# Kernel optimization log

Hardware: AMD Instinct MI355X
Metric: run time of the kernel (lower is better)

Reference implementation:

```python
import jax, jax.numpy as jnp
import numpy as np

B, CIN, H, W = 8, 128, 64, 64
COUT, KH, KW = 128, 3, 3
STRIDE = (1, 1)
PAD = (1, 1)
DIL = (1, 1)
GROUPS = 1
OFFSET_GROUPS = 1

def _out_size(i, k, s, p, d):
    return (i + 2 * p - d * (k - 1) - 1) // s + 1

HO = _out_size(H, KH, STRIDE[0], PAD[0], DIL[0])
WO = _out_size(W, KW, STRIDE[1], PAD[1], DIL[1])


def setup_inputs() -> dict:
    key = jax.random.key(0)
    k1, k2, k3, k4 = jax.random.split(key, 4)
    x = jax.random.normal(k1, (B, CIN, H, W), jnp.float32)
    offset = jax.random.normal(k2, (B, 2 * OFFSET_GROUPS * KH * KW, HO, WO), jnp.float32)
    fan_in = (CIN // GROUPS) * KH * KW
    bound = 1.0 / np.sqrt(fan_in)
    weight = jax.random.uniform(k3, (COUT, CIN // GROUPS, KH, KW), jnp.float32, -bound, bound)
    bias = jax.random.uniform(k4, (COUT,), jnp.float32, -bound, bound)
    return {"x": x, "offset": offset, "weight": weight, "bias": bias}


def _deform_conv2d(x, offset, weight, bias):
    Bn, Cin, Hi, Wi = x.shape
    K = KH * KW
    Goff, Gw = OFFSET_GROUPS, GROUPS
    Cpg = Cin // Goff

    # base sampling positions (before learned offsets)
    ys = jnp.arange(HO, dtype=jnp.float32) * STRIDE[0] - PAD[0]  # [HO]
    xs = jnp.arange(WO, dtype=jnp.float32) * STRIDE[1] - PAD[1]  # [WO]
    base_y = jnp.repeat(jnp.arange(KH, dtype=jnp.float32) * DIL[0], KW)  # [K]
    base_x = jnp.tile(jnp.arange(KW, dtype=jnp.float32) * DIL[1], KH)    # [K]

    # offsets: channel layout is 2*(g*K + k) + {0: dy, 1: dx}
    off = offset.reshape(Bn, Goff, K, 2, HO, WO)
    py = base_y[None, None, :, None, None] + ys[None, None, None, :, None] + off[:, :, :, 0]  # [B,Goff,K,HO,WO]
    px = base_x[None, None, :, None, None] + xs[None, None, None, None, :] + off[:, :, :, 1]

    y0 = jnp.floor(py)
    x0 = jnp.floor(px)
    ly = py - y0  # fractional weights
    lx = px - x0

    xg = x.reshape(Bn, Goff, Cpg, Hi * Wi)

    def gather_one(img, lin):  # img [Cpg, H*W], lin [K,HO,WO] -> [Cpg,K,HO,WO]
        return img[:, lin]

    gather = jax.vmap(jax.vmap(gather_one))  # over B and Goff

    def corner(yi, xi, w):
        # zero-padding semantics: out-of-bounds corner contributes 0
        mask = (yi >= 0) & (yi < Hi) & (xi >= 0) & (xi < Wi)
        iy = jnp.clip(yi, 0, Hi - 1).astype(jnp.int32)
        ix = jnp.clip(xi, 0, Wi - 1).astype(jnp.int32)
        lin = iy * Wi + ix  # [B,Goff,K,HO,WO]
        wm = (w * mask.astype(x.dtype))[:, :, None]  # broadcast over channel axis
        return gather(xg, lin) * wm  # [B,Goff,Cpg,K,HO,WO]

    val = (corner(y0, x0, (1 - ly) * (1 - lx))
           + corner(y0, x0 + 1, (1 - ly) * lx)
           + corner(y0 + 1, x0, ly * (1 - lx))
           + corner(y0 + 1, x0 + 1, ly * lx))  # [B,Goff,Cpg,K,HO,WO]

    # grouped conv accumulate
    val = val.reshape(Bn, Gw, Cin // Gw, K, HO, WO)
    wg = weight.reshape(Gw, COUT // Gw, Cin // Gw, K)
    out = jnp.einsum('bgckhw,gock->bgohw', val, wg).reshape(Bn, COUT, HO, WO)
    return out + bias[None, :, None, None]


def reference(x, offset, weight, bias):
    return _deform_conv2d(x, offset, weight, bias)
```

## Files before the change

### kernel.cpp

```cpp
#include <hip/hip_runtime.h>

typedef unsigned int   u32;
typedef unsigned short u16;
typedef short bf16x8 __attribute__((ext_vector_type(8)));
typedef float f32x4  __attribute__((ext_vector_type(4)));

#define CIN   128
#define COUT  128
#define Hh    64
#define Ww    64
#define Bb    8
#define KPOS  9
#define KDIM  (CIN*KPOS)
#define NKSTEP 36
#define XT_ELEMS (Bb*Hh*Ww*CIN)

__device__ __forceinline__ float bflo(u32 u){ return __uint_as_float(u << 16); }
__device__ __forceinline__ float bfhi(u32 u){ return __uint_as_float(u & 0xffff0000u); }

__device__ __forceinline__ u32 packbf(float a, float b){
    u32 ua = __float_as_uint(a);
    u32 ub = __float_as_uint(b);
    ua += 0x7fffu + ((ua >> 16) & 1u);
    ub += 0x7fffu + ((ub >> 16) & 1u);
    return (ua >> 16) | (ub & 0xffff0000u);
}
__device__ __forceinline__ u16 tobf(float a){
    u32 ua = __float_as_uint(a);
    ua += 0x7fffu + ((ua >> 16) & 1u);
    return (u16)(ua >> 16);
}

__global__ __launch_bounds__(256) void k_transpose(const float* __restrict__ x,
                                                   u16* __restrict__ xT){
    __shared__ float tile[32*33];
    int bi = blockIdx.x;
    int st = bi & 127, ct = (bi >> 7) & 3, b = bi >> 9;
    int sb = st * 32, cb = ct * 32;
    int tid = threadIdx.x;

    int i = tid >> 5, j = tid & 31;
    const float* xp = x + ((size_t)(b*CIN + cb) * 4096) + sb;
#pragma unroll
    for (int rr = 0; rr < 4; ++rr){
        int ci = i + rr*8;
        tile[ci*33 + j] = xp[(size_t)ci*4096 + j];
    }
    __syncthreads();

    int ii = tid >> 4, jj = tid & 15;
    u32* outp = (u32*)xT + ((size_t)b*4096 + sb)*64 + (cb >> 1) + jj;
#pragma unroll
    for (int rr = 0; rr < 2; ++rr){
        int sl = ii + rr*16;
        float v0 = tile[(2*jj  )*33 + sl];
        float v1 = tile[(2*jj+1)*33 + sl];
        outp[(size_t)sl*64] = packbf(v0, v1);
    }
}

__global__ __launch_bounds__(256) void k_wprep(const float* __restrict__ w,
                                               u16* __restrict__ Wt){
    int gid = blockIdx.x*256 + threadIdx.x;
    int jf   = gid & 7;
    int lane = (gid >> 3) & 63;
    int mt   = (gid >> 9) & 7;
    int kt   = gid >> 12;
    int m  = mt*16 + (lane & 15);
    int kk = (lane >> 4)*8 + jf;
    int ck = kt*32 + kk;
    int kpos = ck >> 7;
    int cin  = ck & 127;
    Wt[gid] = tobf(w[((size_t)m*128 + cin)*9 + kpos]);
}

__global__ __launch_bounds__(256, 2)
void k_main(const float* __restrict__ off, const float* __restrict__ bias,
            const u16* __restrict__ xT, const u16* __restrict__ Wt,
            float* __restrict__ out){
    __shared__ u32 Vsm[2][64*20];

    int tid = threadIdx.x;
    int bi  = blockIdx.x;
    int b   = bi & 7;
    int t   = bi >> 3;
    int s0  = t * 64;

    int p  = tid >> 2, qt = tid & 3;
    int ho = t;
    int wo = p;
    const u16* xb_base = xT + (size_t)b * (Hh*Ww*CIN);

    int lane = tid & 63, wave = tid >> 6;
    int wm = wave >> 1, wn = wave & 1;
    int quad = lane >> 4, l16 = lane & 15;

    f32x4 acc[4][2];
#pragma unroll
    for (int i = 0; i < 4; ++i)
#pragma unroll
        for (int j = 0; j < 2; ++j) acc[i][j] = {0.f, 0.f, 0.f, 0.f};

    int   aa[4];
    float wt[4];

    auto state = [&](int kpos){
        int kh = kpos / 3, kw = kpos - kh*3;
        size_t ob = ((size_t)(b*18 + 2*kpos))*4096 + (s0 + p);
        float dy = off[ob];
        float dx = off[ob + 4096];
        float py = (float)(ho + kh - 1) + dy;
        float px = (float)(wo + kw - 1) + dx;
        float y0f = floorf(py), x0f = floorf(px);
        float ly = py - y0f, lx = px - x0f;
        int y0 = (int)y0f, x0 = (int)x0f;
        int y1 = y0 + 1,  x1 = x0 + 1;
        float my0 = (y0 >= 0 && y0 < Hh) ? 1.f : 0.f;
        float my1 = (y1 >= 0 && y1 < Hh) ? 1.f : 0.f;
        float mx0 = (x0 >= 0 && x0 < Ww) ? 1.f : 0.f;
        float mx1 = (x1 >= 0 && x1 < Ww) ? 1.f : 0.f;
        float omly = 1.f - ly, omlx = 1.f - lx;
        wt[0] = omly*omlx*my0*mx0;
        wt[1] = omly*lx  *my0*mx1;
        wt[2] = ly  *omlx*my1*mx0;
        wt[3] = ly  *lx  *my1*mx1;
        int cy0 = min(max(y0,0),Hh-1), cy1 = min(max(y1,0),Hh-1);
        int cx0 = min(max(x0,0),Ww-1), cx1 = min(max(x1,0),Ww-1);
        aa[0] = (cy0*Ww + cx0)*CIN;
        aa[1] = (cy0*Ww + cx1)*CIN;
        aa[2] = (cy1*Ww + cx0)*CIN;
        aa[3] = (cy1*Ww + cx1)*CIN;
    };

    auto gather = [&](int ks, uint4 q[4]){
        int coff = ((ks & 3) << 5) + qt*8;
        const u16* xb = xb_base + coff;
#pragma unroll
        for (int c = 0; c < 4; ++c)
            q[c] = *(const uint4*)(xb + aa[c]);
    };

    auto loadA = [&](int ks, uint4 a[4]){
#pragma unroll
        for (int i = 0; i < 4; ++i)
            a[i] = *(const uint4*)(Wt + (size_t)(((ks*8 + wm*4 + i)*64 + lane))*8);
    };

    auto blend_store = [&](const uint4 q[4], int buf){
        u32 res[4];
#pragma unroll
        for (int d = 0; d < 4; ++d){
            float lo = 0.f, hi = 0.f;
#pragma unroll
            for (int c = 0; c < 4; ++c){
                u32 u = ((const u32*)&q[0])[c*4 + d];
                lo = fmaf(wt[c], bflo(u), lo);
                hi = fmaf(wt[c], bfhi(u), hi);
            }
            res[d] = packbf(lo, hi);
        }
        *(uint4*)&Vsm[buf][p*20 + qt*4] = *(uint4*)&res[0];
    };

    uint4 q[4], araw_cur[4], araw_nxt[4];
    state(0);
    gather(0, q);
    loadA(0, araw_cur);
    blend_store(q, 0);

    for (int ks = 0; ks < NKSTEP; ++ks){
        __syncthreads();
        int nxt = ks + 1;
        bool have_nxt = (nxt < NKSTEP);
        if (have_nxt){
            if ((nxt & 3) == 0) state(nxt >> 2);
            gather(nxt, q);
            loadA(nxt, araw_nxt);
        }

        uint4 braw[2];
#pragma unroll
        for (int j = 0; j < 2; ++j)
            braw[j] = *(const uint4*)&Vsm[ks & 1][((wn*2 + j)*16 + l16)*20 + quad*4];
#pragma unroll
        for (int i = 0; i < 4; ++i){
            bf16x8 av = __builtin_bit_cast(bf16x8, araw_cur[i]);
#pragma unroll
            for (int j = 0; j < 2; ++j){
                bf16x8 bv = __builtin_bit_cast(bf16x8, braw[j]);
                acc[i][j] = __builtin_amdgcn_mfma_f32_16x16x32_bf16(av, bv, acc[i][j], 0, 0, 0);
            }
        }

        if (have_nxt){
            blend_store(q, nxt & 1);
#pragma unroll
            for (int i = 0; i < 4; ++i) araw_cur[i] = araw_nxt[i];
        }
    }

#pragma unroll
    for (int i = 0; i < 4; ++i){
        int cout0 = (wm*4 + i)*16 + quad*4;
#pragma unroll
        for (int j = 0; j < 2; ++j){
            int pcol = (wn*2 + j)*16 + l16;
            size_t obase = ((size_t)(b*COUT + cout0))*4096 + (s0 + pcol);
#pragma unroll
            for (int r = 0; r < 4; ++r){
                out[obase + (size_t)r*4096] = acc[i][j][r] + bias[cout0 + r];
            }
        }
    }
}

extern "C" void kernel_launch(void* const* d_in, const int* in_sizes, int n_in,
                              void* d_out, int out_size, void* d_ws, size_t ws_size,
                              hipStream_t stream){
    const float* x    = (const float*)d_in[0];
    const float* off  = (const float*)d_in[1];
    const float* w    = (const float*)d_in[2];
    const float* bias = (const float*)d_in[3];
    float* out = (float*)d_out;

    u16* xT = (u16*)d_ws;
    u16* Wt = xT + XT_ELEMS;

    k_transpose<<<dim3(4096), dim3(256), 0, stream>>>(x, xT);
    k_wprep    <<<dim3(576),  dim3(256), 0, stream>>>(w, Wt);
    k_main     <<<dim3(512),  dim3(256), 0, stream>>>(off, bias, xT, Wt, out);
}
```

Before: 109.0 us.

## Gather deformable samples directly in MFMA layout, drop LDS and barriers, retile transpose

The main kernel no longer stages blended bilinear samples through double-buffered shared memory. Each lane now gathers and blends the four corners for the two pixels it owns in MFMA B-fragment layout, which removes the per-step __syncthreads and LDS round trip. Offsets, sampling state and gathers are software-pipelined two steps ahead, and the blend uses packed float2 math with a cheaper perm-based bf16 pack. The transpose kernel is retiled to 64x128 tiles with vectorized loads and stores. In exchange, each lane does redundant gathers (every wave gathers its own pixels), register pressure rises, and the bf16 rounding changes from round-to-nearest-even to round-half-up.

```diff
diff --git a/kernel.cpp b/kernel.cpp
--- a/kernel.cpp
+++ b/kernel.cpp
@@ -4,26 +4,23 @@
 typedef unsigned short u16;
 typedef short bf16x8 __attribute__((ext_vector_type(8)));
 typedef float f32x4  __attribute__((ext_vector_type(4)));
+typedef float f32x2  __attribute__((ext_vector_type(2)));
 
 #define CIN   128
 #define COUT  128
 #define Hh    64
 #define Ww    64
 #define Bb    8
-#define KPOS  9
-#define KDIM  (CIN*KPOS)
 #define NKSTEP 36
 #define XT_ELEMS (Bb*Hh*Ww*CIN)
 
 __device__ __forceinline__ float bflo(u32 u){ return __uint_as_float(u << 16); }
 __device__ __forceinline__ float bfhi(u32 u){ return __uint_as_float(u & 0xffff0000u); }
 
-__device__ __forceinline__ u32 packbf(float a, float b){
-    u32 ua = __float_as_uint(a);
-    u32 ub = __float_as_uint(b);
-    ua += 0x7fffu + ((ua >> 16) & 1u);
-    ub += 0x7fffu + ((ub >> 16) & 1u);
-    return (ua >> 16) | (ub & 0xffff0000u);
+__device__ __forceinline__ u32 pack2(float a, float b){
+    u32 lo = __float_as_uint(a) + 0x8000u;
+    u32 hi = __float_as_uint(b) + 0x8000u;
+    return __builtin_amdgcn_perm(hi, lo, 0x07060302u);
 }
 __device__ __forceinline__ u16 tobf(float a){
     u32 ua = __float_as_uint(a);
@@ -33,29 +30,41 @@
 
 __global__ __launch_bounds__(256) void k_transpose(const float* __restrict__ x,
                                                    u16* __restrict__ xT){
-    __shared__ float tile[32*33];
+    __shared__ float lds[64*132];
     int bi = blockIdx.x;
-    int st = bi & 127, ct = (bi >> 7) & 3, b = bi >> 9;
-    int sb = st * 32, cb = ct * 32;
+    int hb = bi & 63, b = bi >> 6;
     int tid = threadIdx.x;
 
-    int i = tid >> 5, j = tid & 31;
-    const float* xp = x + ((size_t)(b*CIN + cb) * 4096) + sb;
-#pragma unroll
-    for (int rr = 0; rr < 4; ++rr){
-        int ci = i + rr*8;
-        tile[ci*33 + j] = xp[(size_t)ci*4096 + j];
+    {
+        int r = tid >> 1, cq = tid & 1;
+        const float* xp = x + ((size_t)(b*128 + r))*4096 + hb*64 + cq*32;
+        float4 v[8];
+#pragma unroll
+        for (int k = 0; k < 8; ++k) v[k] = *(const float4*)(xp + k*4);
+        float* dst = lds + (cq*32)*132 + r;
+#pragma unroll
+        for (int k = 0; k < 8; ++k){
+            dst[(k*4+0)*132] = v[k].x;
+            dst[(k*4+1)*132] = v[k].y;
+            dst[(k*4+2)*132] = v[k].z;
+            dst[(k*4+3)*132] = v[k].w;
+        }
     }
     __syncthreads();
-
-    int ii = tid >> 4, jj = tid & 15;
-    u32* outp = (u32*)xT + ((size_t)b*4096 + sb)*64 + (cb >> 1) + jj;
-#pragma unroll
-    for (int rr = 0; rr < 2; ++rr){
-        int sl = ii + rr*16;
-        float v0 = tile[(2*jj  )*33 + sl];
-        float v1 = tile[(2*jj+1)*33 + sl];
-        outp[(size_t)sl*64] = packbf(v0, v1);
+    {
+        int s = tid >> 2, kq = tid & 3;
+        const float* src = lds + s*132 + kq*32;
+        u32 r16[16];
+#pragma unroll
+        for (int k = 0; k < 8; ++k){
+            float4 v = *(const float4*)(src + k*4);
+            r16[k*2  ] = pack2(v.x, v.y);
+            r16[k*2+1] = pack2(v.z, v.w);
+        }
+        u32* dst = (u32*)xT + ((size_t)(b*4096 + hb*64 + s))*64 + kq*16;
+#pragma unroll
+        for (int k = 0; k < 4; ++k)
+            *(uint4*)(dst + k*4) = *(uint4*)&r16[k*4];
     }
 }
 
@@ -78,125 +87,126 @@
 void k_main(const float* __restrict__ off, const float* __restrict__ bias,
             const u16* __restrict__ xT, const u16* __restrict__ Wt,
             float* __restrict__ out){
-    __shared__ u32 Vsm[2][64*20];
-
-    int tid = threadIdx.x;
-    int bi  = blockIdx.x;
-    int b   = bi & 7;
-    int t   = bi >> 3;
-    int s0  = t * 64;
-
-    int p  = tid >> 2, qt = tid & 3;
-    int ho = t;
-    int wo = p;
-    const u16* xb_base = xT + (size_t)b * (Hh*Ww*CIN);
-
+    int tid = threadIdx.x, bi = blockIdx.x;
+    int b = bi & 7, t = bi >> 3, s0 = t * 64;
     int lane = tid & 63, wave = tid >> 6;
     int wm = wave >> 1, wn = wave & 1;
     int quad = lane >> 4, l16 = lane & 15;
+    int p0 = wn*32 + l16, p1 = p0 + 16;
+
+    const u16* xb = xT + (size_t)b * (4096*128);
+    const float* offb = off + (size_t)b * (18*4096) + s0;
 
     f32x4 acc[4][2];
 #pragma unroll
     for (int i = 0; i < 4; ++i)
 #pragma unroll
-        for (int j = 0; j < 2; ++j) acc[i][j] = {0.f, 0.f, 0.f, 0.f};
-
-    int   aa[4];
-    float wt[4];
-
+        for (int j = 0; j < 2; ++j) acc[i][j] = {0.f,0.f,0.f,0.f};
+
+    int   aaS[2][2][4];
+    float wtS[2][2][4];
+    float4 offv;
+
+    auto load_off = [&](int kpos){
+        const float* op = offb + (size_t)(2*kpos)*4096;
+        offv.x = op[p0]; offv.y = op[4096 + p0];
+        offv.z = op[p1]; offv.w = op[4096 + p1];
+    };
     auto state = [&](int kpos){
-        int kh = kpos / 3, kw = kpos - kh*3;
-        size_t ob = ((size_t)(b*18 + 2*kpos))*4096 + (s0 + p);
-        float dy = off[ob];
-        float dx = off[ob + 4096];
-        float py = (float)(ho + kh - 1) + dy;
-        float px = (float)(wo + kw - 1) + dx;
-        float y0f = floorf(py), x0f = floorf(px);
-        float ly = py - y0f, lx = px - x0f;
-        int y0 = (int)y0f, x0 = (int)x0f;
-        int y1 = y0 + 1,  x1 = x0 + 1;
-        float my0 = (y0 >= 0 && y0 < Hh) ? 1.f : 0.f;
-        float my1 = (y1 >= 0 && y1 < Hh) ? 1.f : 0.f;
-        float mx0 = (x0 >= 0 && x0 < Ww) ? 1.f : 0.f;
-        float mx1 = (x1 >= 0 && x1 < Ww) ? 1.f : 0.f;
-        float omly = 1.f - ly, omlx = 1.f - lx;
-        wt[0] = omly*omlx*my0*mx0;
-        wt[1] = omly*lx  *my0*mx1;
-        wt[2] = ly  *omlx*my1*mx0;
-        wt[3] = ly  *lx  *my1*mx1;
-        int cy0 = min(max(y0,0),Hh-1), cy1 = min(max(y1,0),Hh-1);
-        int cx0 = min(max(x0,0),Ww-1), cx1 = min(max(x1,0),Ww-1);
-        aa[0] = (cy0*Ww + cx0)*CIN;
-        aa[1] = (cy0*Ww + cx1)*CIN;
-        aa[2] = (cy1*Ww + cx0)*CIN;
-        aa[3] = (cy1*Ww + cx1)*CIN;
-    };
-
-    auto gather = [&](int ks, uint4 q[4]){
-        int coff = ((ks & 3) << 5) + qt*8;
-        const u16* xb = xb_base + coff;
-#pragma unroll
-        for (int c = 0; c < 4; ++c)
-            q[c] = *(const uint4*)(xb + aa[c]);
-    };
-
-    auto loadA = [&](int ks, uint4 a[4]){
+        int kh = kpos/3, kw = kpos - kh*3;
+        int st = kpos & 1;
+        float dy[2] = {offv.x, offv.z}, dx[2] = {offv.y, offv.w};
+        int wo[2] = {p0, p1};
+#pragma unroll
+        for (int jt = 0; jt < 2; ++jt){
+            float py = (float)(t + kh - 1) + dy[jt];
+            float px = (float)(wo[jt] + kw - 1) + dx[jt];
+            float y0f = floorf(py), x0f = floorf(px);
+            float ly = py - y0f, lx = px - x0f;
+            int y0 = (int)y0f, x0 = (int)x0f;
+            int y1 = y0 + 1, x1 = x0 + 1;
+            float my0 = (y0>=0 && y0<Hh)?1.f:0.f;
+            float my1 = (y1>=0 && y1<Hh)?1.f:0.f;
+            float mx0 = (x0>=0 && x0<Ww)?1.f:0.f;
+            float mx1 = (x1>=0 && x1<Ww)?1.f:0.f;
+            float oy = 1.f - ly, ox = 1.f - lx;
+            wtS[st][jt][0] = oy*ox*my0*mx0;
+            wtS[st][jt][1] = oy*lx*my0*mx1;
+            wtS[st][jt][2] = ly*ox*my1*mx0;
+            wtS[st][jt][3] = ly*lx*my1*mx1;
+            int cy0 = min(max(y0,0),Hh-1), cy1 = min(max(y1,0),Hh-1);
+            int cx0 = min(max(x0,0),Ww-1), cx1 = min(max(x1,0),Ww-1);
+            aaS[st][jt][0] = (cy0*Ww + cx0)*CIN;
+            aaS[st][jt][1] = (cy0*Ww + cx1)*CIN;
+            aaS[st][jt][2] = (cy1*Ww + cx0)*CIN;
+            aaS[st][jt][3] = (cy1*Ww + cx1)*CIN;
+        }
+    };
+    auto gather = [&](int c, uint4 q[8]){
+        int st = (c >> 2) & 1;
+        const u16* xc = xb + ((c & 3) << 5) + quad*8;
+#pragma unroll
+        for (int jt = 0; jt < 2; ++jt)
+#pragma unroll
+            for (int cc = 0; cc < 4; ++cc)
+                q[jt*4+cc] = *(const uint4*)(xc + aaS[st][jt][cc]);
+    };
+    auto loadA = [&](int c, uint4 a[4]){
+        const u16* wp = Wt + (size_t)((c*8 + wm*4)*64 + lane)*8;
 #pragma unroll
         for (int i = 0; i < 4; ++i)
-            a[i] = *(const uint4*)(Wt + (size_t)(((ks*8 + wm*4 + i)*64 + lane))*8);
-    };
-
-    auto blend_store = [&](const uint4 q[4], int buf){
-        u32 res[4];
-#pragma unroll
-        for (int d = 0; d < 4; ++d){
-            float lo = 0.f, hi = 0.f;
-#pragma unroll
-            for (int c = 0; c < 4; ++c){
-                u32 u = ((const u32*)&q[0])[c*4 + d];
-                lo = fmaf(wt[c], bflo(u), lo);
-                hi = fmaf(wt[c], bfhi(u), hi);
+            a[i] = *(const uint4*)(wp + (size_t)i*64*8);
+    };
+    auto blend = [&](const uint4 q[8], int st, bf16x8 bf[2]){
+#pragma unroll
+        for (int jt = 0; jt < 2; ++jt){
+            u32 r4[4];
+#pragma unroll
+            for (int d = 0; d < 4; ++d){
+                f32x2 s = {0.f, 0.f};
+#pragma unroll
+                for (int c = 0; c < 4; ++c){
+                    u32 u = ((const u32*)q)[(jt*4+c)*4 + d];
+                    f32x2 v = { bflo(u), bfhi(u) };
+                    f32x2 w2 = { wtS[st][jt][c], wtS[st][jt][c] };
+                    s += w2 * v;
+                }
+                r4[d] = pack2(s.x, s.y);
             }
-            res[d] = packbf(lo, hi);
-        }
-        *(uint4*)&Vsm[buf][p*20 + qt*4] = *(uint4*)&res[0];
-    };
-
-    uint4 q[4], araw_cur[4], araw_nxt[4];
+            bf[jt] = *(bf16x8*)&r4[0];
+        }
+    };
+
+    uint4 q[2][8], av[2][4];
+    bf16x8 bf[2];
+    load_off(0);
     state(0);
-    gather(0, q);
-    loadA(0, araw_cur);
-    blend_store(q, 0);
-
+    load_off(1);
+    gather(0, q[0]); loadA(0, av[0]);
+    gather(1, q[1]);
+    blend(q[0], 0, bf);
+
+#pragma unroll 4
     for (int ks = 0; ks < NKSTEP; ++ks){
-        __syncthreads();
-        int nxt = ks + 1;
-        bool have_nxt = (nxt < NKSTEP);
-        if (have_nxt){
-            if ((nxt & 3) == 0) state(nxt >> 2);
-            gather(nxt, q);
-            loadA(nxt, araw_nxt);
-        }
-
-        uint4 braw[2];
-#pragma unroll
-        for (int j = 0; j < 2; ++j)
-            braw[j] = *(const uint4*)&Vsm[ks & 1][((wn*2 + j)*16 + l16)*20 + quad*4];
+        int c1 = ks + 1, c2 = ks + 2;
+        if (c2 < NKSTEP){
+            if ((c2 & 3) == 0){
+                int kp = c2 >> 2;
+                state(kp);
+                if (kp < 8) load_off(kp + 1);
+            }
+            gather(c2, q[c2 & 1]);
+        }
+        if (c1 < NKSTEP) loadA(c1, av[c1 & 1]);
+
 #pragma unroll
         for (int i = 0; i < 4; ++i){
-            bf16x8 av = __builtin_bit_cast(bf16x8, araw_cur[i]);
-#pragma unroll
-            for (int j = 0; j < 2; ++j){
-                bf16x8 bv = __builtin_bit_cast(bf16x8, braw[j]);
-                acc[i][j] = __builtin_amdgcn_mfma_f32_16x16x32_bf16(av, bv, acc[i][j], 0, 0, 0);
-            }
-        }
-
-        if (have_nxt){
-            blend_store(q, nxt & 1);
-#pragma unroll
-            for (int i = 0; i < 4; ++i) araw_cur[i] = araw_nxt[i];
-        }
+            bf16x8 a = *(bf16x8*)&av[ks & 1][i];
+#pragma unroll
+            for (int j = 0; j < 2; ++j)
+                acc[i][j] = __builtin_amdgcn_mfma_f32_16x16x32_bf16(a, bf[j], acc[i][j], 0, 0, 0);
+        }
+        if (c1 < NKSTEP) blend(q[c1 & 1], (c1 >> 2) & 1, bf);
     }
 
 #pragma unroll
@@ -207,9 +217,8 @@
             int pcol = (wn*2 + j)*16 + l16;
             size_t obase = ((size_t)(b*COUT + cout0))*4096 + (s0 + pcol);
 #pragma unroll
-            for (int r = 0; r < 4; ++r){
+            for (int r = 0; r < 4; ++r)
                 out[obase + (size_t)r*4096] = acc[i][j][r] + bias[cout0 + r];
-            }
         }
     }
 }
@@ -226,7 +235,7 @@
     u16* xT = (u16*)d_ws;
     u16* Wt = xT + XT_ELEMS;
 
-    k_transpose<<<dim3(4096), dim3(256), 0, stream>>>(x, xT);
-    k_wprep    <<<dim3(576),  dim3(256), 0, stream>>>(w, Wt);
-    k_main     <<<dim3(512),  dim3(256), 0, stream>>>(off, bias, xT, Wt, out);
-}
+    k_transpose<<<dim3(512), dim3(256), 0, stream>>>(x, xT);
+    k_wprep    <<<dim3(576), dim3(256), 0, stream>>>(w, Wt);
+    k_main     <<<dim3(512), dim3(256), 0, stream>>>(off, bias, xT, Wt, out);
+}
```

Result: slower. 152.0 us (+39.5%).
